# Performance work log

Measured on AMD Instinct MI355X. Metric: run time of the kernel, lower is better.

Reference implementation:

```python
import jax, jax.numpy as jnp
import numpy as np
import math

DIM = 768
HEADS = 12
HEAD_DIM = DIM // HEADS
SCALE_PARAM_INIT = 1.0 / math.sqrt(DIM)  # Scale(scale=1/sqrt(dim), init=1.0)


def cosine_norm(x, eps=1e-6):
    norm = jnp.maximum(jnp.linalg.norm(x, axis=-1, keepdims=True), eps)
    return x / norm


def setup_inputs() -> dict:
    key = jax.random.key(0)
    ks = jax.random.split(key, 6)
    B, N = 8, 1024
    x = jax.random.normal(ks[0], (B, N, DIM), dtype=jnp.float32)
    # torch nn.Linear weights are [out, in]; y = x @ W^T
    std = 1.0 / math.sqrt(DIM)
    Wq = jax.random.uniform(ks[1], (DIM, DIM), jnp.float32, -std, std)
    Wk = jax.random.uniform(ks[2], (DIM, DIM), jnp.float32, -std, std)
    Wv = jax.random.uniform(ks[3], (DIM, DIM), jnp.float32, -std, std)
    Wo = jax.random.uniform(ks[4], (DIM, DIM), jnp.float32, -std, std)
    # Scale param s: ones * scale, perturbed slightly for generality
    s_qk = SCALE_PARAM_INIT * (1.0 + 0.1 * jax.random.normal(ks[5], (HEADS, HEAD_DIM), jnp.float32))
    return {"x": x, "Wq": Wq, "Wk": Wk, "Wv": Wv, "Wo": Wo, "s_qk": s_qk}


def reference(x, Wq, Wk, Wv, Wo, s_qk):
    B, N, _ = x.shape
    # projections (torch Linear: x @ W^T)
    q = (x @ Wq.T).reshape(B, N, HEADS, HEAD_DIM)
    k = (x @ Wk.T).reshape(B, N, HEADS, HEAD_DIM)
    v = (x @ Wv.T).reshape(B, N, HEADS, HEAD_DIM)
    # effective scale = s * (init / scale)
    s_eff = s_qk * (1.0 / SCALE_PARAM_INIT)  # [H, D]
    q = cosine_norm(q) * s_eff  # broadcast over [B, N, H, D]
    k = cosine_norm(k) * s_eff
    scale = HEAD_DIM ** 0.5  # note: multiplies logits (nGPT-style)
    # [B, H, N, N]
    logits = jnp.einsum('bqhd,bkhd->bhqk', q, k) * scale
    attn = jax.nn.softmax(logits, axis=-1)
    out = jnp.einsum('bhqk,bkhd->bqhd', attn, v).reshape(B, N, HEADS * HEAD_DIM)
    return out @ Wo.T
```

## Files before the change

kernel.cpp:

```cpp
#include <hip/hip_runtime.h>
#include <hip/hip_bf16.h>
#include <math.h>

#define NDIM 768
#define NHEADS 12
#define HD 64
#define SEQ 1024
#define BATCH 8
#define MROWS (BATCH * SEQ)
#define SQRT_DIM 27.712812921102035f
#define LOG2E 1.4426950408889634f

typedef unsigned short u16;
typedef unsigned int u32;
typedef __attribute__((ext_vector_type(8))) short short8;
typedef __attribute__((ext_vector_type(4))) short bf16x4;
typedef __attribute__((ext_vector_type(4))) float f32x4;
typedef __attribute__((ext_vector_type(16))) float f32x16;
typedef __attribute__((ext_vector_type(2))) u32 u32x2;
typedef __attribute__((ext_vector_type(4))) u32 u32x4;

#define MFMA16(a, b, c) __builtin_amdgcn_mfma_f32_16x16x32_bf16(a, b, c, 0, 0, 0)
#define MFMA32(a, b, c) __builtin_amdgcn_mfma_f32_32x32x16_bf16(a, b, c, 0, 0, 0)

#if __has_builtin(__builtin_amdgcn_exp2f)
#define EXP2(x) __builtin_amdgcn_exp2f(x)
#else
#define EXP2(x) exp2f(x)
#endif

__device__ inline u16 f2bf(float f) {
    __hip_bfloat16 h = __float2bfloat16(f);
    return *reinterpret_cast<u16*>(&h);
}

__device__ inline u32 rne_pack(float a, float b) {
    u32 ua = __builtin_bit_cast(u32, a), ub = __builtin_bit_cast(u32, b);
    ua = (ua + 0x7fffu + ((ua >> 16) & 1u)) >> 16;
    ub = (ub + 0x7fffu + ((ub >> 16) & 1u)) >> 16;
    return (ub << 16) | ua;
}

__device__ inline u32 cvtpk(float a, float b) {
    u32 r;
    asm("v_cvt_pk_bf16_f32 %0, %1, %2" : "=v"(r) : "v"(a), "v"(b));
    return r;
}

__device__ inline void gl2lds16(const void* g, void* l) {
    __builtin_amdgcn_global_load_lds((const __attribute__((address_space(1))) void*)g,
                                     (__attribute__((address_space(3))) void*)l, 16, 0, 0);
}

__device__ inline void bar() {
    asm volatile("" ::: "memory");
    __builtin_amdgcn_s_barrier();
    asm volatile("" ::: "memory");
}
#define LGKM0 asm volatile("s_waitcnt lgkmcnt(0)" ::: "memory")
#define VM0   asm volatile("s_waitcnt vmcnt(0)" ::: "memory")

__device__ inline void plswap(u32 a, u32 b, int half, u32& x, u32& y) {
#if __has_builtin(__builtin_amdgcn_permlane32_swap)
    u32x2 r = __builtin_amdgcn_permlane32_swap(a, b, false, false);
    x = r[0]; y = r[1];
#else
    u32 oa = __shfl_xor(a, 32, 64), ob = __shfl_xor(b, 32, 64);
    x = half ? ob : a;
    y = half ? b : oa;
#endif
}

__global__ __launch_bounds__(256) void castall(const float* __restrict__ x,
                                               const float* __restrict__ Wq,
                                               const float* __restrict__ Wk,
                                               const float* __restrict__ Wv,
                                               const float* __restrict__ Wo,
                                               u16* __restrict__ xb,
                                               u16* __restrict__ Wqkv,
                                               u16* __restrict__ Wob) {
    const int WB = (NDIM * NDIM) / 1024;
    int blk = blockIdx.x;
    const float* s;
    u16* d;
    int base;
    if (blk < 6144) {
        s = x; d = xb; base = blk * 1024;
    } else {
        int wsel = (blk - 6144) / WB, r = (blk - 6144) % WB;
        base = r * 1024;
        if (wsel == 0)      { s = Wq; d = Wqkv; }
        else if (wsel == 1) { s = Wk; d = Wqkv + NDIM * NDIM; }
        else if (wsel == 2) { s = Wv; d = Wqkv + 2 * NDIM * NDIM; }
        else                { s = Wo; d = Wob; }
    }
    int i = base + threadIdx.x * 4;
    float4 v = *(const float4*)(s + i);
    uint2 o = make_uint2(rne_pack(v.x, v.y), rne_pack(v.z, v.w));
    *(uint2*)(d + i) = o;
}

__global__ __launch_bounds__(512, 2) void gemm256_qkv(const u16* __restrict__ A,
                                                      const u16* __restrict__ B,
                                                      u16* __restrict__ Vt,
                                                      const float* __restrict__ s_qk,
                                                      u16* __restrict__ Qdst,
                                                      u16* __restrict__ Kdst) {
    constexpr int K = NDIM;
    constexpr int NT = K / 64;
    __shared__ __align__(16) u16 As[2][2][128 * 64];
    __shared__ __align__(16) u16 Bs[2][2][128 * 64];

    const int t = threadIdx.x;
    const int wave = t >> 6, lane = t & 63;
    const int quad = lane >> 4, l16 = lane & 15;
    const int fx = l16 & 7;
    const int blk = blockIdx.x;

    const int srow = lane >> 3;
    const int schk = (lane & 7) ^ srow;
    auto stg = [&](const u16* src, u16* dst) {
#pragma unroll
        for (int it = 0; it < 2; ++it) {
            const int cb = it * 512 + wave * 64;
            const int r = (cb >> 3) + srow;
            gl2lds16(src + (size_t)r * K + schk * 8, (char*)dst + cb * 16);
        }
    };

    if (blk < 256) {
        const int wm = wave >> 2, wn = wave & 3;
        const int xcd = blk & 7, local = blk >> 3;
        const int bm = xcd * 1024 + (local >> 3) * 256;
        const int bn = (local & 7) * 256;

        f32x4 acc[8][4];
#pragma unroll
        for (int i = 0; i < 8; ++i)
#pragma unroll
            for (int j = 0; j < 4; ++j) acc[i][j] = (f32x4){0.f, 0.f, 0.f, 0.f};

        const u16* Ag = A + (size_t)bm * K;
        const u16* Bg = B + (size_t)bn * K;

        stg(Ag,                        As[0][0]);
        stg(Ag + (size_t)128 * K,      As[0][1]);
        stg(Bg,                        Bs[0][0]);
        stg(Bg + (size_t)128 * K,      Bs[0][1]);
        stg(Bg + 64,                   Bs[1][0]);
        stg(Bg + (size_t)128 * K + 64, Bs[1][1]);
        asm volatile("s_waitcnt vmcnt(4)" ::: "memory");
        bar();

        short8 a[4][2], b0[2][2], b1[2][2];
        const int rb0 = (wn & 1) * 64;

#pragma unroll 2
        for (int T = 0; T < NT; ++T) {
            const int db = T & 1;
            u16* Asl = As[db][wm];
            u16* Bsl = Bs[db][wn >> 1];
            const u16* An = Ag + (size_t)(T + 1) * 64;
            const u16* Bn = Bg + (size_t)(T + 2) * 64;

#pragma unroll
            for (int mi = 0; mi < 4; ++mi) {
                const int r = mi * 16 + l16;
#pragma unroll
                for (int kk = 0; kk < 2; ++kk)
                    a[mi][kk] = *(const short8*)&Asl[(r * 8 + ((kk * 4 + quad) ^ fx)) * 8];
            }
#pragma unroll
            for (int ni = 0; ni < 2; ++ni) {
                const int r = rb0 + ni * 16 + l16;
#pragma unroll
                for (int kk = 0; kk < 2; ++kk)
                    b0[ni][kk] = *(const short8*)&Bsl[(r * 8 + ((kk * 4 + quad) ^ fx)) * 8];
            }
            if (T + 1 < NT) stg(An, As[db ^ 1][0]);
            bar();
            LGKM0;
            __builtin_amdgcn_s_setprio(1);
#pragma unroll
            for (int kk = 0; kk < 2; ++kk)
#pragma unroll
                for (int mi = 0; mi < 4; ++mi)
#pragma unroll
                    for (int ni = 0; ni < 2; ++ni)
                        acc[mi][ni] = MFMA16(a[mi][kk], b0[ni][kk], acc[mi][ni]);
            __builtin_amdgcn_s_setprio(0);
            bar();

#pragma unroll
            for (int ni = 0; ni < 2; ++ni) {
                const int r = rb0 + (ni + 2) * 16 + l16;
#pragma unroll
                for (int kk = 0; kk < 2; ++kk)
                    b1[ni][kk] = *(const short8*)&Bsl[(r * 8 + ((kk * 4 + quad) ^ fx)) * 8];
            }
            if (T + 1 < NT) stg(An + (size_t)128 * K, As[db ^ 1][1]);
            bar();
            LGKM0;
            __builtin_amdgcn_s_setprio(1);
#pragma unroll
            for (int kk = 0; kk < 2; ++kk)
#pragma unroll
                for (int mi = 0; mi < 4; ++mi)
#pragma unroll
                    for (int ni = 0; ni < 2; ++ni)
                        acc[mi][ni + 2] = MFMA16(a[mi][kk], b1[ni][kk], acc[mi][ni + 2]);
            __builtin_amdgcn_s_setprio(0);
            bar();

#pragma unroll
            for (int mi = 0; mi < 4; ++mi) {
                const int r = (mi + 4) * 16 + l16;
#pragma unroll
                for (int kk = 0; kk < 2; ++kk)
                    a[mi][kk] = *(const short8*)&Asl[(r * 8 + ((kk * 4 + quad) ^ fx)) * 8];
            }
            if (T + 2 < NT) stg(Bn, Bs[db][0]);
            bar();
            LGKM0;
            __builtin_amdgcn_s_setprio(1);
#pragma unroll
            for (int kk = 0; kk < 2; ++kk)
#pragma unroll
                for (int mi = 0; mi < 4; ++mi)
#pragma unroll
                    for (int ni = 0; ni < 2; ++ni)
                        acc[mi + 4][ni + 2] = MFMA16(a[mi][kk], b1[ni][kk], acc[mi + 4][ni + 2]);
            __builtin_amdgcn_s_setprio(0);
            bar();

            if (T + 2 < NT) stg(Bn + (size_t)128 * K, Bs[db][1]);
            bar();
            __builtin_amdgcn_s_setprio(1);
#pragma unroll
            for (int kk = 0; kk < 2; ++kk)
#pragma unroll
                for (int mi = 0; mi < 4; ++mi)
#pragma unroll
                    for (int ni = 0; ni < 2; ++ni)
                        acc[mi + 4][ni] = MFMA16(a[mi][kk], b0[ni][kk], acc[mi + 4][ni]);
            __builtin_amdgcn_s_setprio(0);
            if (T + 2 < NT) {
                asm volatile("s_waitcnt vmcnt(4)" ::: "memory");
            } else {
                VM0;
            }
            bar();
        }

        const int cg = (bn + wn * 64) >> 6;
        if (cg >= 2 * NHEADS) {
            const int h = cg - 2 * NHEADS;
#pragma unroll
            for (int mi = 0; mi < 8; ++mi) {
                const int row = bm + wm * 128 + mi * 16 + quad * 4;
                const int bb = row >> 10, n0 = row & 1023;
#pragma unroll
                for (int ni = 0; ni < 4; ++ni) {
                    const int dd = ni * 16 + l16;
                    uint2 pk = make_uint2(rne_pack(acc[mi][ni][0], acc[mi][ni][1]),
                                          rne_pack(acc[mi][ni][2], acc[mi][ni][3]));
                    *(uint2*)(Vt + (((size_t)(bb * NHEADS + h) * HD + dd) << 10) + n0) = pk;
                }
            }
        } else {
            const bool isq = cg < NHEADS;
            const int h = isq ? cg : cg - NHEADS;
            u16* dst = isq ? Qdst : Kdst;
            const float ex = isq ? 8.f * LOG2E : 1.f;
            float sq[4];
#pragma unroll
            for (int ni = 0; ni < 4; ++ni)
                sq[ni] = s_qk[h * HD + ni * 16 + l16] * SQRT_DIM * ex;
#pragma unroll
            for (int mi = 0; mi < 8; ++mi)
#pragma unroll
                for (int r = 0; r < 4; ++r) {
                    float ss = 0.f;
#pragma unroll
                    for (int ni = 0; ni < 4; ++ni) ss += acc[mi][ni][r] * acc[mi][ni][r];
                    ss += __shfl_xor(ss, 1, 64);
                    ss += __shfl_xor(ss, 2, 64);
                    ss += __shfl_xor(ss, 4, 64);
                    ss += __shfl_xor(ss, 8, 64);
                    float inv = 1.f / fmaxf(sqrtf(ss), 1e-6f);
                    const int row = bm + wm * 128 + mi * 16 + quad * 4 + r;
                    const int bb = row >> 10, tok = row & 1023;
                    u16* o = dst + ((size_t)(bb * NHEADS + h) * SEQ + tok) * HD;
#pragma unroll
                    for (int ni = 0; ni < 4; ++ni)
                        o[ni * 16 + l16] = f2bf(acc[mi][ni][r] * sq[ni] * inv);
                }
        }
    } else {
        const int q = blk - 256;
        const int bm = (q >> 1) * 128;
        const int bn = 2048 + (q & 1) * 128;
        const int wm4 = wave >> 1, wn2 = wave & 1;
        const u16* Aq = A + (size_t)bm * K;
        const u16* Bq = B + (size_t)bn * K;

        f32x4 qa[2][4];
#pragma unroll
        for (int i = 0; i < 2; ++i)
#pragma unroll
            for (int j = 0; j < 4; ++j) qa[i][j] = (f32x4){0.f, 0.f, 0.f, 0.f};

        stg(Aq, As[0][0]);
        stg(Bq, Bs[0][0]);
        VM0;
        bar();
#pragma unroll 2
        for (int T = 0; T < NT; ++T) {
            const int db = T & 1;
            if (T + 1 < NT) {
                stg(Aq + (size_t)(T + 1) * 64, As[db ^ 1][0]);
                stg(Bq + (size_t)(T + 1) * 64, Bs[db ^ 1][0]);
            }
            const u16* Asl = As[db][0];
            const u16* Bsl = Bs[db][0];
            short8 af[2][2], bf[4][2];
#pragma unroll
            for (int mi = 0; mi < 2; ++mi) {
                const int r = wm4 * 32 + mi * 16 + l16;
#pragma unroll
                for (int kk = 0; kk < 2; ++kk)
                    af[mi][kk] = *(const short8*)&Asl[(r * 8 + ((kk * 4 + quad) ^ fx)) * 8];
            }
#pragma unroll
            for (int ni = 0; ni < 4; ++ni) {
                const int r = wn2 * 64 + ni * 16 + l16;
#pragma unroll
                for (int kk = 0; kk < 2; ++kk)
                    bf[ni][kk] = *(const short8*)&Bsl[(r * 8 + ((kk * 4 + quad) ^ fx)) * 8];
            }
            __builtin_amdgcn_s_setprio(1);
#pragma unroll
            for (int kk = 0; kk < 2; ++kk)
#pragma unroll
                for (int mi = 0; mi < 2; ++mi)
#pragma unroll
                    for (int ni = 0; ni < 4; ++ni)
                        qa[mi][ni] = MFMA16(af[mi][kk], bf[ni][kk], qa[mi][ni]);
            __builtin_amdgcn_s_setprio(0);
            VM0;
            bar();
        }
        const int h = 8 + (q & 1) * 2 + wn2;
#pragma unroll
        for (int mi = 0; mi < 2; ++mi) {
            const int row = bm + wm4 * 32 + mi * 16 + quad * 4;
            const int bb = row >> 10, n0 = row & 1023;
#pragma unroll
            for (int ni = 0; ni < 4; ++ni) {
                const int dd = ni * 16 + l16;
                uint2 pk = make_uint2(rne_pack(qa[mi][ni][0], qa[mi][ni][1]),
                                      rne_pack(qa[mi][ni][2], qa[mi][ni][3]));
                *(uint2*)(Vt + (((size_t)(bb * NHEADS + h) * HD + dd) << 10) + n0) = pk;
            }
        }
    }
}

template <int EPI>
__global__ __launch_bounds__(256) void gemm_bf16(const u16* __restrict__ A,
                                                 const u16* __restrict__ B,
                                                 void* __restrict__ C, int N,
                                                 const float* __restrict__ s_qk,
                                                 u16* __restrict__ Qdst,
                                                 u16* __restrict__ Kdst,
                                                 int NX) {
    constexpr int K = NDIM;
    constexpr int NKT = K / 32;
    __shared__ __align__(16) u16 As[2][4096];
    __shared__ __align__(16) u16 Bs[2][4096];
    const int t = threadIdx.x;
    const int wave = t >> 6, lane = t & 63;
    const int quad = lane >> 4, l16 = lane & 15;
    const int wx = (wave & 1) * 64, wy = (wave >> 1) * 64;
    const int blk = blockIdx.x;
    const int xcd = blk & 7, local = blk >> 3;
    const int bm = (xcd * 8 + local / NX) * 128;
    const int bn = (local % NX) * 128;

    f32x4 acc[4][4];
#pragma unroll
    for (int i = 0; i < 4; ++i)
#pragma unroll
        for (int j = 0; j < 4; ++j) acc[i][j] = (f32x4){0.f, 0.f, 0.f, 0.f};

    const int srl = lane >> 2;
    const int skc = (lane & 3) ^ ((lane >> 3) & 3);
    auto stage = [&](int k0, int bsel) {
#pragma unroll
        for (int it = 0; it < 2; ++it) {
            const int cb = it * 256 + wave * 64;
            const int row = (cb >> 6) * 16 + srl;
            gl2lds16(A + (size_t)(bm + row) * K + k0 + skc * 8,
                     (char*)As[bsel] + cb * 16);
            gl2lds16(B + (size_t)(bn + row) * K + k0 + skc * 8,
                     (char*)Bs[bsel] + cb * 16);
        }
    };
    const int fxor = (l16 >> 1) & 3;

    stage(0, 0);
#pragma unroll
    for (int kt = 0; kt < NKT; ++kt) {
        __syncthreads();
        if (kt + 1 < NKT) stage((kt + 1) * 32, (kt + 1) & 1);
        const int b = kt & 1;
        short8 af[4], bfr[4];
#pragma unroll
        for (int i = 0; i < 4; ++i)
            af[i] = *(const short8*)&As[b][
                ((((wy >> 4) + i) * 64 + l16 * 4 + (quad ^ fxor)) * 8)];
#pragma unroll
        for (int j = 0; j < 4; ++j)
            bfr[j] = *(const short8*)&Bs[b][
                ((((wx >> 4) + j) * 64 + l16 * 4 + (quad ^ fxor)) * 8)];
#pragma unroll
        for (int i = 0; i < 4; ++i)
#pragma unroll
            for (int j = 0; j < 4; ++j) acc[i][j] = MFMA16(af[i], bfr[j], acc[i][j]);
    }

    if constexpr (EPI == 0) {
#pragma unroll
        for (int i = 0; i < 4; ++i)
#pragma unroll
            for (int j = 0; j < 4; ++j)
#pragma unroll
                for (int r = 0; r < 4; ++r) {
                    const int row = bm + wy + i * 16 + quad * 4 + r;
                    const int col = bn + wx + j * 16 + l16;
                    ((float*)C)[(size_t)row * N + col] = acc[i][j][r];
                }
    }
}

__global__ __launch_bounds__(256, 3) void attn_mfma(const u16* __restrict__ Qh,
                                                    const u16* __restrict__ Kh,
                                                    const u16* __restrict__ Vt,
                                                    u16* __restrict__ AO) {
    __shared__ __align__(16) u16 Ks[2][512 * 8];
    __shared__ __align__(16) u16 Vs[2][512 * 8];

    const int t = threadIdx.x;
    const int wave = t >> 6, lane = t & 63;
    const int l31 = lane & 31, half = lane >> 5;

    const int bid = blockIdx.x;
    const int xcd = bid & 7, idx = bid >> 3;
    const int bh = xcd * 12 + (idx % 12);
    const int q0 = (idx / 12) * 128;
    const int b = bh / NHEADS, h = bh - b * NHEADS;

    const u16* Kb = Kh + (size_t)bh * SEQ * HD;
    const u16* Vb = Vt + (size_t)bh * HD * SEQ;
    const int qb = q0 + wave * 32;

    short8 qf[4];
#pragma unroll
    for (int tt = 0; tt < 4; ++tt)
        qf[tt] = *(const short8*)(Qh + ((size_t)bh * SEQ + qb + l31) * HD +
                                  tt * 16 + half * 8);

    f32x16 o[2];
#pragma unroll
    for (int dt = 0; dt < 2; ++dt)
#pragma unroll
        for (int r = 0; r < 16; ++r) o[dt][r] = 0.f;
    float lp = 0.f;

    const int arl = lane >> 3;
    const int acc8 = (lane & 7) ^ arl;
    const int fx8 = l31 & 7;

    auto stage = [&](int j0, int db) {
#pragma unroll
        for (int it = 0; it < 2; ++it) {
            const int cb = it * 256 + wave * 64;
            const int r0 = (cb >> 6) * 8 + arl;
            gl2lds16(Kb + (size_t)(j0 + r0) * HD + acc8 * 8,
                     (char*)Ks[db] + cb * 16);
            gl2lds16(Vb + (size_t)r0 * SEQ + j0 + acc8 * 8,
                     (char*)Vs[db] + cb * 16);
        }
    };

    stage(0, 0);
#pragma unroll 2
    for (int jt = 0; jt < SEQ / 64; ++jt) {
        const int db = jt & 1;
        VM0;
        bar();
        if (jt + 1 < SEQ / 64) stage((jt + 1) * 64, db ^ 1);
        const u16* Ksl = Ks[db];
        const u16* Vsl = Vs[db];

        f32x16 sa0, sa1;
#pragma unroll
        for (int r = 0; r < 16; ++r) { sa0[r] = 0.f; sa1[r] = 0.f; }
#pragma unroll
        for (int tt = 0; tt < 4; ++tt) {
            short8 kf0 = *(const short8*)&Ksl[
                ((((l31 >> 3)) * 64) + fx8 * 8 + ((2 * tt + half) ^ fx8)) * 8];
            short8 kf1 = *(const short8*)&Ksl[
                (((4 + (l31 >> 3)) * 64) + fx8 * 8 + ((2 * tt + half) ^ fx8)) * 8];
            sa0 = MFMA32(kf0, qf[tt], sa0);
            sa1 = MFMA32(kf1, qf[tt], sa1);
        }

        short8 pf0a, pf0b, pf1a, pf1b;
        {
            float p[16];
#pragma unroll
            for (int r = 0; r < 16; ++r) p[r] = EXP2(sa0[r]);
#pragma unroll
            for (int rg = 0; rg < 4; ++rg)
                lp += (p[rg * 4] + p[rg * 4 + 1]) + (p[rg * 4 + 2] + p[rg * 4 + 3]);
            u32 q[8];
#pragma unroll
            for (int i = 0; i < 8; ++i) q[i] = cvtpk(p[2 * i], p[2 * i + 1]);
            u32 d0, d1, d2, d3, e0, e1, e2, e3;
            plswap(q[0], q[2], half, d0, d2);
            plswap(q[1], q[3], half, d1, d3);
            plswap(q[4], q[6], half, e0, e2);
            plswap(q[5], q[7], half, e1, e3);
            u32x4 f0v = {d0, d1, d2, d3};
            u32x4 f1v = {e0, e1, e2, e3};
            pf0a = __builtin_bit_cast(short8, f0v);
            pf0b = __builtin_bit_cast(short8, f1v);
        }
        {
            float p[16];
#pragma unroll
            for (int r = 0; r < 16; ++r) p[r] = EXP2(sa1[r]);
#pragma unroll
            for (int rg = 0; rg < 4; ++rg)
                lp += (p[rg * 4] + p[rg * 4 + 1]) + (p[rg * 4 + 2] + p[rg * 4 + 3]);
            u32 q[8];
#pragma unroll
            for (int i = 0; i < 8; ++i) q[i] = cvtpk(p[2 * i], p[2 * i + 1]);
            u32 d0, d1, d2, d3, e0, e1, e2, e3;
            plswap(q[0], q[2], half, d0, d2);
            plswap(q[1], q[3], half, d1, d3);
            plswap(q[4], q[6], half, e0, e2);
            plswap(q[5], q[7], half, e1, e3);
            u32x4 f0v = {d0, d1, d2, d3};
            u32x4 f1v = {e0, e1, e2, e3};
            pf1a = __builtin_bit_cast(short8, f0v);
            pf1b = __builtin_bit_cast(short8, f1v);
        }

#pragma unroll
        for (int kt = 0; kt < 2; ++kt)
#pragma unroll
            for (int s = 0; s < 2; ++s) {
                short8 pf = kt ? (s ? pf1b : pf1a) : (s ? pf0b : pf0a);
                const int c = kt * 4 + s * 2 + half;
#pragma unroll
                for (int dt = 0; dt < 2; ++dt) {
                    short8 vf = *(const short8*)&Vsl[
                        (((dt * 4 + (l31 >> 3)) * 64) + fx8 * 8 + (c ^ fx8)) * 8];
                    o[dt] = MFMA32(vf, pf, o[dt]);
                }
            }
    }

    const float invl = 1.f / (lp + __shfl_xor(lp, 32, 64));
    u16* ob = AO + (size_t)(b * SEQ + qb + l31) * NDIM + h * HD;
#pragma unroll
    for (int dt = 0; dt < 2; ++dt)
#pragma unroll
        for (int rg = 0; rg < 4; ++rg) {
            bf16x4 ok = {(short)f2bf(o[dt][rg * 4 + 0] * invl),
                         (short)f2bf(o[dt][rg * 4 + 1] * invl),
                         (short)f2bf(o[dt][rg * 4 + 2] * invl),
                         (short)f2bf(o[dt][rg * 4 + 3] * invl)};
            *(bf16x4*)(ob + dt * 32 + rg * 8 + half * 4) = ok;
        }
}

extern "C" void kernel_launch(void* const* d_in, const int* in_sizes, int n_in,
                              void* d_out, int out_size, void* d_ws, size_t ws_size,
                              hipStream_t stream) {
    const float* x    = (const float*)d_in[0];
    const float* Wq   = (const float*)d_in[1];
    const float* Wk   = (const float*)d_in[2];
    const float* Wv   = (const float*)d_in[3];
    const float* Wo   = (const float*)d_in[4];
    const float* s_qk = (const float*)d_in[5];
    float* out = (float*)d_out;

    char* w = (char*)d_ws;
    const size_t TE = (size_t)MROWS * NDIM;
    u16* xb   = (u16*)w;                    w += TE * 2;
    u16* Wqkv = (u16*)w;                    w += (size_t)3 * NDIM * NDIM * 2;
    u16* Wob  = (u16*)w;                    w += (size_t)NDIM * NDIM * 2;
    u16* Qh   = (u16*)w;                    w += TE * 2;
    u16* Kh   = (u16*)w;                    w += TE * 2;
    u16* Vt   = (u16*)w;                    w += TE * 2;
    u16* ao   = (u16*)w;

    castall<<<6144 + 4 * 576, 256, 0, stream>>>(x, Wq, Wk, Wv, Wo, xb, Wqkv, Wob);

    gemm256_qkv<<<384, 512, 0, stream>>>(xb, Wqkv, Vt, s_qk, Qh, Kh);

    attn_mfma<<<768, 256, 0, stream>>>(Qh, Kh, Vt, ao);

    gemm_bf16<0><<<6 * 64, 256, 0, stream>>>(
        ao, Wob, out, NDIM, nullptr, nullptr, nullptr, 6);
}
```

Before: 179.2 us.

## Fold leftover V-projection tiles into main QKV GEMM blocks, drop tail blocks

The QKV GEMM previously launched 256 large 256x256 blocks plus 128 smaller blocks to cover the last 256 output columns (V heads 8-11). Now each large block also computes a 32x256 slice of those remaining columns. It reuses its already-staged A tile from LDS and reads the B fragments for those columns directly from global memory. This removes the second wave of tail blocks and the load imbalance they cause on a 256-CU device. In exchange it adds extra MFMAs, register pressure and uncoalesced global B loads inside the main loop.

```diff
diff --git a/kernel.cpp b/kernel.cpp
--- a/kernel.cpp
+++ b/kernel.cpp
@@ -128,240 +128,207 @@
         }
     };
 
-    if (blk < 256) {
-        const int wm = wave >> 2, wn = wave & 3;
-        const int xcd = blk & 7, local = blk >> 3;
-        const int bm = xcd * 1024 + (local >> 3) * 256;
-        const int bn = (local & 7) * 256;
-
-        f32x4 acc[8][4];
-#pragma unroll
-        for (int i = 0; i < 8; ++i)
-#pragma unroll
-            for (int j = 0; j < 4; ++j) acc[i][j] = (f32x4){0.f, 0.f, 0.f, 0.f};
-
-        const u16* Ag = A + (size_t)bm * K;
-        const u16* Bg = B + (size_t)bn * K;
-
-        stg(Ag,                        As[0][0]);
-        stg(Ag + (size_t)128 * K,      As[0][1]);
-        stg(Bg,                        Bs[0][0]);
-        stg(Bg + (size_t)128 * K,      Bs[0][1]);
-        stg(Bg + 64,                   Bs[1][0]);
-        stg(Bg + (size_t)128 * K + 64, Bs[1][1]);
-        asm volatile("s_waitcnt vmcnt(4)" ::: "memory");
-        bar();
-
-        short8 a[4][2], b0[2][2], b1[2][2];
-        const int rb0 = (wn & 1) * 64;
+    const int wm = wave >> 2, wn = wave & 3;
+    const int xcd = blk & 7, local = blk >> 3;
+    const int bm = xcd * 1024 + (local >> 3) * 256;
+    const int bn = (local & 7) * 256;
+    const int nt = local & 7;
+
+    f32x4 acc[8][4];
+#pragma unroll
+    for (int i = 0; i < 8; ++i)
+#pragma unroll
+        for (int j = 0; j < 4; ++j) acc[i][j] = (f32x4){0.f, 0.f, 0.f, 0.f};
+    f32x4 accs[4];
+#pragma unroll
+    for (int j = 0; j < 4; ++j) accs[j] = (f32x4){0.f, 0.f, 0.f, 0.f};
+
+    const u16* Ag = A + (size_t)bm * K;
+    const u16* Bg = B + (size_t)bn * K;
+    const int srow_s = nt * 32 + wm * 16;
+    const int svhalf = srow_s >> 7;
+    const int slr = (srow_s & 127) + l16;
+    const u16* Bsv = B + (size_t)(2048 + wn * 64 + l16) * K;
+
+    stg(Ag,                        As[0][0]);
+    stg(Ag + (size_t)128 * K,      As[0][1]);
+    stg(Bg,                        Bs[0][0]);
+    stg(Bg + (size_t)128 * K,      Bs[0][1]);
+    stg(Bg + 64,                   Bs[1][0]);
+    stg(Bg + (size_t)128 * K + 64, Bs[1][1]);
+    asm volatile("s_waitcnt vmcnt(4)" ::: "memory");
+    bar();
+
+    short8 a[4][2], b0[2][2], b1[2][2];
+    short8 sa_[2], sb_[4][2];
+    const int rb0 = (wn & 1) * 64;
 
 #pragma unroll 2
-        for (int T = 0; T < NT; ++T) {
-            const int db = T & 1;
-            u16* Asl = As[db][wm];
-            u16* Bsl = Bs[db][wn >> 1];
-            const u16* An = Ag + (size_t)(T + 1) * 64;
-            const u16* Bn = Bg + (size_t)(T + 2) * 64;
-
-#pragma unroll
-            for (int mi = 0; mi < 4; ++mi) {
-                const int r = mi * 16 + l16;
-#pragma unroll
-                for (int kk = 0; kk < 2; ++kk)
-                    a[mi][kk] = *(const short8*)&Asl[(r * 8 + ((kk * 4 + quad) ^ fx)) * 8];
-            }
-#pragma unroll
-            for (int ni = 0; ni < 2; ++ni) {
-                const int r = rb0 + ni * 16 + l16;
-#pragma unroll
-                for (int kk = 0; kk < 2; ++kk)
-                    b0[ni][kk] = *(const short8*)&Bsl[(r * 8 + ((kk * 4 + quad) ^ fx)) * 8];
-            }
-            if (T + 1 < NT) stg(An, As[db ^ 1][0]);
-            bar();
-            LGKM0;
-            __builtin_amdgcn_s_setprio(1);
+    for (int T = 0; T < NT; ++T) {
+        const int db = T & 1;
+        u16* Asl = As[db][wm];
+        u16* Bsl = Bs[db][wn >> 1];
+        const u16* An = Ag + (size_t)(T + 1) * 64;
+        const u16* Bn = Bg + (size_t)(T + 2) * 64;
+
+#pragma unroll
+        for (int ni = 0; ni < 4; ++ni)
 #pragma unroll
             for (int kk = 0; kk < 2; ++kk)
-#pragma unroll
-                for (int mi = 0; mi < 4; ++mi)
-#pragma unroll
-                    for (int ni = 0; ni < 2; ++ni)
-                        acc[mi][ni] = MFMA16(a[mi][kk], b0[ni][kk], acc[mi][ni]);
-            __builtin_amdgcn_s_setprio(0);
-            bar();
-
-#pragma unroll
-            for (int ni = 0; ni < 2; ++ni) {
-                const int r = rb0 + (ni + 2) * 16 + l16;
-#pragma unroll
-                for (int kk = 0; kk < 2; ++kk)
-                    b1[ni][kk] = *(const short8*)&Bsl[(r * 8 + ((kk * 4 + quad) ^ fx)) * 8];
-            }
-            if (T + 1 < NT) stg(An + (size_t)128 * K, As[db ^ 1][1]);
-            bar();
-            LGKM0;
-            __builtin_amdgcn_s_setprio(1);
+                sb_[ni][kk] = *(const short8*)(Bsv + (size_t)ni * 16 * K +
+                                               T * 64 + (kk * 4 + quad) * 8);
+#pragma unroll
+        for (int mi = 0; mi < 4; ++mi) {
+            const int r = mi * 16 + l16;
 #pragma unroll
             for (int kk = 0; kk < 2; ++kk)
-#pragma unroll
-                for (int mi = 0; mi < 4; ++mi)
-#pragma unroll
-                    for (int ni = 0; ni < 2; ++ni)
-                        acc[mi][ni + 2] = MFMA16(a[mi][kk], b1[ni][kk], acc[mi][ni + 2]);
-            __builtin_amdgcn_s_setprio(0);
-            bar();
-
-#pragma unroll
-            for (int mi = 0; mi < 4; ++mi) {
-                const int r = (mi + 4) * 16 + l16;
-#pragma unroll
-                for (int kk = 0; kk < 2; ++kk)
-                    a[mi][kk] = *(const short8*)&Asl[(r * 8 + ((kk * 4 + quad) ^ fx)) * 8];
-            }
-            if (T + 2 < NT) stg(Bn, Bs[db][0]);
-            bar();
-            LGKM0;
-            __builtin_amdgcn_s_setprio(1);
+                a[mi][kk] = *(const short8*)&Asl[(r * 8 + ((kk * 4 + quad) ^ fx)) * 8];
+        }
+#pragma unroll
+        for (int ni = 0; ni < 2; ++ni) {
+            const int r = rb0 + ni * 16 + l16;
 #pragma unroll
             for (int kk = 0; kk < 2; ++kk)
-#pragma unroll
-                for (int mi = 0; mi < 4; ++mi)
-#pragma unroll
-                    for (int ni = 0; ni < 2; ++ni)
-                        acc[mi + 4][ni + 2] = MFMA16(a[mi][kk], b1[ni][kk], acc[mi + 4][ni + 2]);
-            __builtin_amdgcn_s_setprio(0);
-            bar();
-
-            if (T + 2 < NT) stg(Bn + (size_t)128 * K, Bs[db][1]);
-            bar();
-            __builtin_amdgcn_s_setprio(1);
+                b0[ni][kk] = *(const short8*)&Bsl[(r * 8 + ((kk * 4 + quad) ^ fx)) * 8];
+        }
+#pragma unroll
+        for (int kk = 0; kk < 2; ++kk)
+            sa_[kk] = *(const short8*)&As[db][svhalf][
+                (slr * 8 + ((kk * 4 + quad) ^ fx)) * 8];
+        if (T + 1 < NT) stg(An, As[db ^ 1][0]);
+        bar();
+        LGKM0;
+        __builtin_amdgcn_s_setprio(1);
+#pragma unroll
+        for (int kk = 0; kk < 2; ++kk)
+#pragma unroll
+            for (int mi = 0; mi < 4; ++mi)
+#pragma unroll
+                for (int ni = 0; ni < 2; ++ni)
+                    acc[mi][ni] = MFMA16(a[mi][kk], b0[ni][kk], acc[mi][ni]);
+        __builtin_amdgcn_s_setprio(0);
+        bar();
+
+#pragma unroll
+        for (int ni = 0; ni < 2; ++ni) {
+            const int r = rb0 + (ni + 2) * 16 + l16;
 #pragma unroll
             for (int kk = 0; kk < 2; ++kk)
-#pragma unroll
-                for (int mi = 0; mi < 4; ++mi)
-#pragma unroll
-                    for (int ni = 0; ni < 2; ++ni)
-                        acc[mi + 4][ni] = MFMA16(a[mi][kk], b0[ni][kk], acc[mi + 4][ni]);
-            __builtin_amdgcn_s_setprio(0);
-            if (T + 2 < NT) {
-                asm volatile("s_waitcnt vmcnt(4)" ::: "memory");
-            } else {
-                VM0;
-            }
-            bar();
-        }
-
-        const int cg = (bn + wn * 64) >> 6;
-        if (cg >= 2 * NHEADS) {
-            const int h = cg - 2 * NHEADS;
-#pragma unroll
-            for (int mi = 0; mi < 8; ++mi) {
-                const int row = bm + wm * 128 + mi * 16 + quad * 4;
-                const int bb = row >> 10, n0 = row & 1023;
-#pragma unroll
-                for (int ni = 0; ni < 4; ++ni) {
-                    const int dd = ni * 16 + l16;
-                    uint2 pk = make_uint2(rne_pack(acc[mi][ni][0], acc[mi][ni][1]),
-                                          rne_pack(acc[mi][ni][2], acc[mi][ni][3]));
-                    *(uint2*)(Vt + (((size_t)(bb * NHEADS + h) * HD + dd) << 10) + n0) = pk;
-                }
-            }
+                b1[ni][kk] = *(const short8*)&Bsl[(r * 8 + ((kk * 4 + quad) ^ fx)) * 8];
+        }
+        if (T + 1 < NT) stg(An + (size_t)128 * K, As[db ^ 1][1]);
+        bar();
+        LGKM0;
+        __builtin_amdgcn_s_setprio(1);
+#pragma unroll
+        for (int kk = 0; kk < 2; ++kk)
+#pragma unroll
+            for (int mi = 0; mi < 4; ++mi)
+#pragma unroll
+                for (int ni = 0; ni < 2; ++ni)
+                    acc[mi][ni + 2] = MFMA16(a[mi][kk], b1[ni][kk], acc[mi][ni + 2]);
+#pragma unroll
+        for (int kk = 0; kk < 2; ++kk)
+#pragma unroll
+            for (int ni = 0; ni < 4; ++ni)
+                accs[ni] = MFMA16(sa_[kk], sb_[ni][kk], accs[ni]);
+        __builtin_amdgcn_s_setprio(0);
+        bar();
+
+#pragma unroll
+        for (int mi = 0; mi < 4; ++mi) {
+            const int r = (mi + 4) * 16 + l16;
+#pragma unroll
+            for (int kk = 0; kk < 2; ++kk)
+                a[mi][kk] = *(const short8*)&Asl[(r * 8 + ((kk * 4 + quad) ^ fx)) * 8];
+        }
+        if (T + 2 < NT) stg(Bn, Bs[db][0]);
+        bar();
+        LGKM0;
+        __builtin_amdgcn_s_setprio(1);
+#pragma unroll
+        for (int kk = 0; kk < 2; ++kk)
+#pragma unroll
+            for (int mi = 0; mi < 4; ++mi)
+#pragma unroll
+                for (int ni = 0; ni < 2; ++ni)
+                    acc[mi + 4][ni + 2] = MFMA16(a[mi][kk], b1[ni][kk], acc[mi + 4][ni + 2]);
+        __builtin_amdgcn_s_setprio(0);
+        bar();
+
+        if (T + 2 < NT) stg(Bn + (size_t)128 * K, Bs[db][1]);
+        bar();
+        __builtin_amdgcn_s_setprio(1);
+#pragma unroll
+        for (int kk = 0; kk < 2; ++kk)
+#pragma unroll
+            for (int mi = 0; mi < 4; ++mi)
+#pragma unroll
+                for (int ni = 0; ni < 2; ++ni)
+                    acc[mi + 4][ni] = MFMA16(a[mi][kk], b0[ni][kk], acc[mi + 4][ni]);
+        __builtin_amdgcn_s_setprio(0);
+        if (T + 2 < NT) {
+            asm volatile("s_waitcnt vmcnt(4)" ::: "memory");
         } else {
-            const bool isq = cg < NHEADS;
-            const int h = isq ? cg : cg - NHEADS;
-            u16* dst = isq ? Qdst : Kdst;
-            const float ex = isq ? 8.f * LOG2E : 1.f;
-            float sq[4];
-#pragma unroll
-            for (int ni = 0; ni < 4; ++ni)
-                sq[ni] = s_qk[h * HD + ni * 16 + l16] * SQRT_DIM * ex;
-#pragma unroll
-            for (int mi = 0; mi < 8; ++mi)
-#pragma unroll
-                for (int r = 0; r < 4; ++r) {
-                    float ss = 0.f;
-#pragma unroll
-                    for (int ni = 0; ni < 4; ++ni) ss += acc[mi][ni][r] * acc[mi][ni][r];
-                    ss += __shfl_xor(ss, 1, 64);
-                    ss += __shfl_xor(ss, 2, 64);
-                    ss += __shfl_xor(ss, 4, 64);
-                    ss += __shfl_xor(ss, 8, 64);
-                    float inv = 1.f / fmaxf(sqrtf(ss), 1e-6f);
-                    const int row = bm + wm * 128 + mi * 16 + quad * 4 + r;
-                    const int bb = row >> 10, tok = row & 1023;
-                    u16* o = dst + ((size_t)(bb * NHEADS + h) * SEQ + tok) * HD;
-#pragma unroll
-                    for (int ni = 0; ni < 4; ++ni)
-                        o[ni * 16 + l16] = f2bf(acc[mi][ni][r] * sq[ni] * inv);
-                }
-        }
-    } else {
-        const int q = blk - 256;
-        const int bm = (q >> 1) * 128;
-        const int bn = 2048 + (q & 1) * 128;
-        const int wm4 = wave >> 1, wn2 = wave & 1;
-        const u16* Aq = A + (size_t)bm * K;
-        const u16* Bq = B + (size_t)bn * K;
-
-        f32x4 qa[2][4];
-#pragma unroll
-        for (int i = 0; i < 2; ++i)
-#pragma unroll
-            for (int j = 0; j < 4; ++j) qa[i][j] = (f32x4){0.f, 0.f, 0.f, 0.f};
-
-        stg(Aq, As[0][0]);
-        stg(Bq, Bs[0][0]);
-        VM0;
-        bar();
-#pragma unroll 2
-        for (int T = 0; T < NT; ++T) {
-            const int db = T & 1;
-            if (T + 1 < NT) {
-                stg(Aq + (size_t)(T + 1) * 64, As[db ^ 1][0]);
-                stg(Bq + (size_t)(T + 1) * 64, Bs[db ^ 1][0]);
-            }
-            const u16* Asl = As[db][0];
-            const u16* Bsl = Bs[db][0];
-            short8 af[2][2], bf[4][2];
-#pragma unroll
-            for (int mi = 0; mi < 2; ++mi) {
-                const int r = wm4 * 32 + mi * 16 + l16;
-#pragma unroll
-                for (int kk = 0; kk < 2; ++kk)
-                    af[mi][kk] = *(const short8*)&Asl[(r * 8 + ((kk * 4 + quad) ^ fx)) * 8];
-            }
-#pragma unroll
-            for (int ni = 0; ni < 4; ++ni) {
-                const int r = wn2 * 64 + ni * 16 + l16;
-#pragma unroll
-                for (int kk = 0; kk < 2; ++kk)
-                    bf[ni][kk] = *(const short8*)&Bsl[(r * 8 + ((kk * 4 + quad) ^ fx)) * 8];
-            }
-            __builtin_amdgcn_s_setprio(1);
-#pragma unroll
-            for (int kk = 0; kk < 2; ++kk)
-#pragma unroll
-                for (int mi = 0; mi < 2; ++mi)
-#pragma unroll
-                    for (int ni = 0; ni < 4; ++ni)
-                        qa[mi][ni] = MFMA16(af[mi][kk], bf[ni][kk], qa[mi][ni]);
-            __builtin_amdgcn_s_setprio(0);
             VM0;
-            bar();
-        }
-        const int h = 8 + (q & 1) * 2 + wn2;
-#pragma unroll
-        for (int mi = 0; mi < 2; ++mi) {
-            const int row = bm + wm4 * 32 + mi * 16 + quad * 4;
+        }
+        bar();
+    }
+
+    const int cg = (bn + wn * 64) >> 6;
+    if (cg >= 2 * NHEADS) {
+        const int h = cg - 2 * NHEADS;
+#pragma unroll
+        for (int mi = 0; mi < 8; ++mi) {
+            const int row = bm + wm * 128 + mi * 16 + quad * 4;
             const int bb = row >> 10, n0 = row & 1023;
 #pragma unroll
             for (int ni = 0; ni < 4; ++ni) {
                 const int dd = ni * 16 + l16;
-                uint2 pk = make_uint2(rne_pack(qa[mi][ni][0], qa[mi][ni][1]),
-                                      rne_pack(qa[mi][ni][2], qa[mi][ni][3]));
+                uint2 pk = make_uint2(rne_pack(acc[mi][ni][0], acc[mi][ni][1]),
+                                      rne_pack(acc[mi][ni][2], acc[mi][ni][3]));
                 *(uint2*)(Vt + (((size_t)(bb * NHEADS + h) * HD + dd) << 10) + n0) = pk;
             }
+        }
+    } else {
+        const bool isq = cg < NHEADS;
+        const int h = isq ? cg : cg - NHEADS;
+        u16* dst = isq ? Qdst : Kdst;
+        const float ex = isq ? 8.f * LOG2E : 1.f;
+        float sq[4];
+#pragma unroll
+        for (int ni = 0; ni < 4; ++ni)
+            sq[ni] = s_qk[h * HD + ni * 16 + l16] * SQRT_DIM * ex;
+#pragma unroll
+        for (int mi = 0; mi < 8; ++mi)
+#pragma unroll
+            for (int r = 0; r < 4; ++r) {
+                float ss = 0.f;
+#pragma unroll
+                for (int ni = 0; ni < 4; ++ni) ss += acc[mi][ni][r] * acc[mi][ni][r];
+                ss += __shfl_xor(ss, 1, 64);
+                ss += __shfl_xor(ss, 2, 64);
+                ss += __shfl_xor(ss, 4, 64);
+                ss += __shfl_xor(ss, 8, 64);
+                float inv = 1.f / fmaxf(sqrtf(ss), 1e-6f);
+                const int row = bm + wm * 128 + mi * 16 + quad * 4 + r;
+                const int bb = row >> 10, tok = row & 1023;
+                u16* o = dst + ((size_t)(bb * NHEADS + h) * SEQ + tok) * HD;
+#pragma unroll
+                for (int ni = 0; ni < 4; ++ni)
+                    o[ni * 16 + l16] = f2bf(acc[mi][ni][r] * sq[ni] * inv);
+            }
+    }
+    {
+        const int row0 = bm + nt * 32 + wm * 16 + quad * 4;
+        const int bb = row0 >> 10, n0 = row0 & 1023;
+#pragma unroll
+        for (int ni = 0; ni < 4; ++ni) {
+            const int cv = wn * 64 + ni * 16 + l16;
+            const int h = 8 + (cv >> 6), dd = cv & 63;
+            uint2 pk = make_uint2(rne_pack(accs[ni][0], accs[ni][1]),
+                                  rne_pack(accs[ni][2], accs[ni][3]));
+            *(uint2*)(Vt + (((size_t)(bb * NHEADS + h) * HD + dd) << 10) + n0) = pk;
         }
     }
 }
@@ -610,7 +577,7 @@
 
     castall<<<6144 + 4 * 576, 256, 0, stream>>>(x, Wq, Wk, Wv, Wo, xb, Wqkv, Wob);
 
-    gemm256_qkv<<<384, 512, 0, stream>>>(xb, Wqkv, Vt, s_qk, Qh, Kh);
+    gemm256_qkv<<<256, 512, 0, stream>>>(xb, Wqkv, Vt, s_qk, Qh, Kh);
 
     attn_mfma<<<768, 256, 0, stream>>>(Qh, Kh, Vt, ao);
 
```

Result: slower. 235.9 us (+31.6%).
